# Performance work log

Measured on AMD Instinct MI355X. Metric: run time of the kernel, lower is better.

## Reference

```python
import jax, jax.numpy as jnp
import numpy as np

LAM = 0.9
Z_MAX = 5.0


def setup_inputs() -> dict:
    key = jax.random.key(0)
    d2 = jax.random.uniform(key, (32, 2048, 512), dtype=jnp.float32)
    return {"d2": d2}


def reference(d2):
    # d2: (B, L, K). Leaky-integrator (EMA) over time with clamp to [0, Z_MAX].
    B, L, K = d2.shape
    one_minus = 1.0 - LAM

    def step(z_t, d2_t):
        z_t = jnp.clip(LAM * z_t + one_minus * d2_t, 0.0, Z_MAX)
        return z_t, z_t

    z0 = jnp.zeros((B, K), dtype=d2.dtype)
    # scan over time axis: move L to leading axis
    _, z = jax.lax.scan(step, z0, jnp.moveaxis(d2, 1, 0))
    return jnp.moveaxis(z, 0, 1)  # (B, L, K)
```

## Files before the change

kernel.cpp:

```cpp
#include <hip/hip_runtime.h>


typedef float f32x4 __attribute__((ext_vector_type(4)));

constexpr int B  = 32;
constexpr int L  = 2048;
constexpr int K  = 512;
constexpr int KV = K / 4;
constexpr int NC = 16;
constexpr int C  = L / NC;
constexpr int W  = 64;

__global__ __launch_bounds__(256)
void ema_chunk_v4_kernel(const f32x4* __restrict__ d2, f32x4* __restrict__ out) {
    const float lam = 0.9f, om = 0.1f, zmax = 5.0f;

    int tid = blockIdx.x * blockDim.x + threadIdx.x;
    int k4  = tid & (KV - 1);
    int bc  = tid >> 7;
    int c   = bc & (NC - 1);
    int b   = bc >> 4;

    const f32x4* in = d2  + (size_t)b * L * KV + k4;
    f32x4*       o  = out + (size_t)b * L * KV + k4;

    int t0 = c * C;
    int tw = t0 - W;
    if (tw < 0) tw = 0;

    float z0 = 0.0f, z1 = 0.0f, z2 = 0.0f, z3 = 0.0f;

    #pragma unroll 8
    for (int t = tw; t < t0; ++t) {
        f32x4 d = in[(size_t)t * KV];
        z0 = fminf(fmaxf(lam * z0 + om * d.x, 0.0f), zmax);
        z1 = fminf(fmaxf(lam * z1 + om * d.y, 0.0f), zmax);
        z2 = fminf(fmaxf(lam * z2 + om * d.z, 0.0f), zmax);
        z3 = fminf(fmaxf(lam * z3 + om * d.w, 0.0f), zmax);
    }

    #pragma unroll 8
    for (int t = t0; t < t0 + C; ++t) {
        f32x4 d = in[(size_t)t * KV];
        z0 = fminf(fmaxf(lam * z0 + om * d.x, 0.0f), zmax);
        z1 = fminf(fmaxf(lam * z1 + om * d.y, 0.0f), zmax);
        z2 = fminf(fmaxf(lam * z2 + om * d.z, 0.0f), zmax);
        z3 = fminf(fmaxf(lam * z3 + om * d.w, 0.0f), zmax);
        f32x4 r = {z0, z1, z2, z3};
        __builtin_nontemporal_store(r, &o[(size_t)t * KV]);
    }
}

extern "C" void kernel_launch(void* const* d_in, const int* in_sizes, int n_in,
                              void* d_out, int out_size, void* d_ws, size_t ws_size,
                              hipStream_t stream) {
    const f32x4* d2 = (const f32x4*)d_in[0];
    f32x4* out = (f32x4*)d_out;

    int total = B * NC * KV;
    int block = 256;
    int grid  = total / block;
    ema_chunk_v4_kernel<<<grid, block, 0, stream>>>(d2, out);
}
```

Before: 54.44 us.

## Use float2 per thread to double thread count, unroll 16, plain stores

Each thread now handles two channels with float2 loads instead of four with float4, which doubles the number of threads and waves available to hide memory latency across the time-chunked EMA scan. Unrolling goes from 8 to 16 and the nontemporal store becomes a regular store. In exchange, each memory instruction moves half as many bytes, so more instructions are issued per byte. Output writes may also pollute the cache more without the nontemporal hint.

```diff
diff --git a/kernel.cpp b/kernel.cpp
--- a/kernel.cpp
+++ b/kernel.cpp
@@ -1,64 +1,60 @@
 #include <hip/hip_runtime.h>
 
 
-typedef float f32x4 __attribute__((ext_vector_type(4)));
+typedef float f32x2 __attribute__((ext_vector_type(2)));
 
-constexpr int B  = 32;
-constexpr int L  = 2048;
-constexpr int K  = 512;
-constexpr int KV = K / 4;
-constexpr int NC = 16;
-constexpr int C  = L / NC;
-constexpr int W  = 64;
+constexpr int B   = 32;
+constexpr int L   = 2048;
+constexpr int K   = 512;
+constexpr int KV2 = K / 2;
+constexpr int NC  = 16;
+constexpr int C   = L / NC;
+constexpr int W   = 64;
 
 __global__ __launch_bounds__(256)
-void ema_chunk_v4_kernel(const f32x4* __restrict__ d2, f32x4* __restrict__ out) {
+void ema_chunk_v2_kernel(const f32x2* __restrict__ d2, f32x2* __restrict__ out) {
     const float lam = 0.9f, om = 0.1f, zmax = 5.0f;
 
     int tid = blockIdx.x * blockDim.x + threadIdx.x;
-    int k4  = tid & (KV - 1);
-    int bc  = tid >> 7;
+    int k2  = tid & (KV2 - 1);
+    int bc  = tid >> 8;
     int c   = bc & (NC - 1);
     int b   = bc >> 4;
 
-    const f32x4* in = d2  + (size_t)b * L * KV + k4;
-    f32x4*       o  = out + (size_t)b * L * KV + k4;
+    const f32x2* in = d2  + (size_t)b * L * KV2 + k2;
+    f32x2*       o  = out + (size_t)b * L * KV2 + k2;
 
     int t0 = c * C;
     int tw = t0 - W;
     if (tw < 0) tw = 0;
 
-    float z0 = 0.0f, z1 = 0.0f, z2 = 0.0f, z3 = 0.0f;
+    float z0 = 0.0f, z1 = 0.0f;
 
-    #pragma unroll 8
+    #pragma unroll 16
     for (int t = tw; t < t0; ++t) {
-        f32x4 d = in[(size_t)t * KV];
+        f32x2 d = in[(size_t)t * KV2];
         z0 = fminf(fmaxf(lam * z0 + om * d.x, 0.0f), zmax);
         z1 = fminf(fmaxf(lam * z1 + om * d.y, 0.0f), zmax);
-        z2 = fminf(fmaxf(lam * z2 + om * d.z, 0.0f), zmax);
-        z3 = fminf(fmaxf(lam * z3 + om * d.w, 0.0f), zmax);
     }
 
-    #pragma unroll 8
+    #pragma unroll 16
     for (int t = t0; t < t0 + C; ++t) {
-        f32x4 d = in[(size_t)t * KV];
+        f32x2 d = in[(size_t)t * KV2];
         z0 = fminf(fmaxf(lam * z0 + om * d.x, 0.0f), zmax);
         z1 = fminf(fmaxf(lam * z1 + om * d.y, 0.0f), zmax);
-        z2 = fminf(fmaxf(lam * z2 + om * d.z, 0.0f), zmax);
-        z3 = fminf(fmaxf(lam * z3 + om * d.w, 0.0f), zmax);
-        f32x4 r = {z0, z1, z2, z3};
-        __builtin_nontemporal_store(r, &o[(size_t)t * KV]);
+        f32x2 r = {z0, z1};
+        o[(size_t)t * KV2] = r;
     }
 }
 
 extern "C" void kernel_launch(void* const* d_in, const int* in_sizes, int n_in,
                               void* d_out, int out_size, void* d_ws, size_t ws_size,
                               hipStream_t stream) {
-    const f32x4* d2 = (const f32x4*)d_in[0];
-    f32x4* out = (f32x4*)d_out;
+    const f32x2* d2 = (const f32x2*)d_in[0];
+    f32x2* out = (f32x2*)d_out;
 
-    int total = B * NC * KV;
+    int total = B * NC * KV2;
     int block = 256;
     int grid  = total / block;
-    ema_chunk_v4_kernel<<<grid, block, 0, stream>>>(d2, out);
+    ema_chunk_v2_kernel<<<grid, block, 0, stream>>>(d2, out);
 }
```

New measurement: 53.60 us. About the same (-1.5%).
